# Kernel tuning notes

Measured on AMD Instinct MI355X. Metric: run time of the kernel, lower is better.

The kernel has to match this reference:

```python
import jax, jax.numpy as jnp
import numpy as np
import math

V = 32768; H = 768; NH = 12; D = 64; L = 12; I = 2048
S = 512; B = 8; BK = 32; MAXP = 512; EPS = 1e-7
STD = math.sqrt(2.0 / (5.0 * H))
SCALE = 1.0 / math.sqrt(3 * D)


def _bucket_positions(seq_len):
    # static numpy: DeBERTa-style log-bucketed relative positions
    rel = np.arange(seq_len)[:, None] - np.arange(seq_len)[None, :]
    sign = np.sign(rel)
    mid = BK // 2
    abs_pos = np.where((rel < mid) & (rel > -mid), mid - 1, np.minimum(np.abs(rel), MAXP - 1))
    log_pos = np.ceil(np.log(abs_pos / mid) / math.log((MAXP - 1) / mid) * (mid - 1)).astype(np.int64) + mid
    bucket = np.where(abs_pos <= mid, rel, log_pos * sign).astype(np.int64)
    return bucket + BK - 1  # [S, S] in [0, 2*BK-2]


def _ln(x):
    # LayerNorm without affine params (elementwise_affine=False)
    m = jnp.mean(x, axis=-1, keepdims=True)
    v = jnp.var(x, axis=-1, keepdims=True)
    return (x - m) * jax.lax.rsqrt(v + EPS)


def _forward(input_ids, attention_mask, word_emb, rel_emb, rel_g, rel_b,
             Wqk, bqk, Wvg, bvg, Wout, bout, W1, W2):
    pos_idx = jnp.asarray(_bucket_positions(S))      # [S, S]
    x = _ln(word_emb[input_ids])                     # [S, B, H]
    rel = _ln(rel_emb) * rel_g + rel_b               # [2*BK-1, H] (affine LN)
    mask = attention_mask                            # [B, 1, 1, S] bool, True = masked
    for i in range(L):
        # ---- disentangled attention ----
        hs = _ln(x)
        qk = jnp.einsum('sbh,oh->sbo', hs, Wqk[i]) + bqk[i]
        q, k = jnp.split(qk, 2, axis=-1)
        vg = jnp.einsum('sbh,oh->sbo', hs, Wvg[i]) + bvg[i]
        v, g = jnp.split(vg, 2, axis=-1)
        g = jax.nn.gelu(g, approximate=False)
        pos = jnp.einsum('rh,oh->ro', rel, Wqk[i]) + bqk[i]   # [2*BK-1, 2H]
        posg = pos[pos_idx]                                   # [S, S, 2H]
        qpos, kpos = jnp.split(posg, 2, axis=-1)
        qpos = qpos.reshape(S, S, NH, D)
        kpos = kpos.reshape(S, S, NH, D)
        qh = q.reshape(S, B, NH, D)
        kh = k.reshape(S, B, NH, D)
        vh = v.reshape(S, B, NH, D)
        scores = jnp.einsum('qbhd,kbhd->bhqk', qh, kh) * SCALE          # content-content
        scores = scores + jnp.einsum('qbhd,qkhd->bhqk', qh, kpos) * SCALE  # content-position
        scores = scores + jnp.einsum('kbhd,qkhd->bhqk', kh, qpos) * SCALE  # position-content
        s = jnp.where(mask, -1e9, scores)
        p = jax.nn.softmax(s, axis=-1)
        p = jnp.where(mask, 0.0, p)
        ctx = jnp.einsum('bhqk,kbhd->qbhd', p, vh).reshape(S, B, H)
        ctx = _ln(ctx * g)
        ctx = jnp.einsum('sbh,oh->sbo', ctx, Wout[i]) + bout[i]
        x = x + ctx
        # ---- GeGLU feed-forward ----
        h = _ln(x)
        h = jnp.einsum('sbh,oh->sbo', h, W1[i])   # [S, B, 2I]
        a, gt = jnp.split(h, 2, axis=-1)
        h = _ln(a * jax.nn.gelu(gt, approximate=True))
        h = jnp.einsum('sbi,oi->sbo', h, W2[i])
        x = x + h
    return x


def setup_inputs() -> dict:
    key = jax.random.key(0)
    ks = jax.random.split(key, 12)
    def nrm(k, shape):
        return (jax.random.normal(k, shape) * STD).astype(jnp.float32)
    return {
        'input_ids': jax.random.randint(ks[0], (S, B), 0, V),
        'attention_mask': jax.random.randint(ks[1], (B, 1, 1, S), 0, 2).astype(bool),
        'word_emb': nrm(ks[2], (V, H)),
        'rel_emb': nrm(ks[3], (2 * BK - 1, H)),
        'rel_g': jnp.ones((H,), jnp.float32),
        'rel_b': jnp.zeros((H,), jnp.float32),
        'Wqk': nrm(ks[4], (L, 2 * H, H)),
        'bqk': jnp.zeros((L, 2 * H), jnp.float32),
        'Wvg': nrm(ks[5], (L, 2 * H, H)),
        'bvg': jnp.zeros((L, 2 * H), jnp.float32),
        'Wout': nrm(ks[6], (L, H, H)),
        'bout': jnp.zeros((L, H), jnp.float32),
        'W1': nrm(ks[7], (L, 2 * I, H)),
        'W2': nrm(ks[8], (L, H, I)),
    }


def reference(input_ids, attention_mask, word_emb, rel_emb, rel_g, rel_b,
              Wqk, bqk, Wvg, bvg, Wout, bout, W1, W2):
    return _forward(input_ids, attention_mask, word_emb, rel_emb, rel_g, rel_b,
                    Wqk, bqk, Wvg, bvg, Wout, bout, W1, W2)
```

## Files before the change

kernel.cpp:

```cpp
#include <hip/hip_runtime.h>
#include <math.h>

#define SS 512
#define BB 8
#define NHH 12
#define DD 64
#define HH 768
#define II 2048
#define LL 12
#define SCALE_F 0.07216878364870323f

typedef __attribute__((ext_vector_type(8))) short bf16x8;
typedef __attribute__((ext_vector_type(4))) float f32x4;

__device__ __forceinline__ unsigned short f2b(float f) {
    union { float f; unsigned int u; } x; x.f = f;
    unsigned int r = x.u + 0x7fffu + ((x.u >> 16) & 1u);
    return (unsigned short)(r >> 16);
}
__device__ __forceinline__ float b2f(unsigned short u) {
    union { unsigned int u; float f; } x; x.u = ((unsigned int)u) << 16;
    return x.f;
}

__device__ __forceinline__ float2 blockReduceSum2(float a, float b) {
    __shared__ float2 sm[4];
    __shared__ float2 bc;
#pragma unroll
    for (int o = 32; o > 0; o >>= 1) {
        a += __shfl_down(a, o);
        b += __shfl_down(b, o);
    }
    int t = threadIdx.x;
    if ((t & 63) == 0) sm[t >> 6] = make_float2(a, b);
    __syncthreads();
    if (t == 0) {
        float xa = sm[0].x + sm[1].x + sm[2].x + sm[3].x;
        float xb = sm[0].y + sm[1].y + sm[2].y + sm[3].y;
        bc = make_float2(xa, xb);
    }
    __syncthreads();
    return bc;
}

__device__ __forceinline__ float gelu_erf(float v) {
    return 0.5f * v * (1.0f + erff(v * 0.70710678118654752f));
}
__device__ __forceinline__ float gelu_tanh(float v) {
    const float c = 0.7978845608028654f;
    return 0.5f * v * (1.0f + tanhf(c * (v + 0.044715f * v * v * v)));
}

__global__ __launch_bounds__(256) void k_decode_mask(const unsigned char* __restrict__ raw,
                                                     int* __restrict__ mask, int n) {
    __shared__ int s_any;
    if (threadIdx.x == 0) s_any = 0;
    __syncthreads();
    int local = 0;
    for (int i = threadIdx.x; i < n; i += blockDim.x)
        if ((i & 3) && raw[i]) local = 1;
    if (local) atomicOr(&s_any, 1);
    __syncthreads();
    bool isU8 = (s_any != 0);
    const int* as_int = (const int*)raw;
    for (int i = threadIdx.x; i < n; i += blockDim.x)
        mask[i] = isU8 ? (raw[i] != 0) : (as_int[i] != 0);
}

__global__ __launch_bounds__(256) void k_bucket(int* __restrict__ tab) {
    int i = blockIdx.x * 256 + threadIdx.x;
    if (i >= 1023) return;
    int rel = i - 511;
    int a = rel < 0 ? -rel : rel;
    int abs_pos = (a < 16) ? 15 : (a < 511 ? a : 511);
    int bucket;
    if (abs_pos <= 16) {
        bucket = rel;
    } else {
        double lp = ceil(log((double)abs_pos / 16.0) / log(511.0 / 16.0) * 15.0);
        int l = (int)lp + 16;
        bucket = (rel > 0) ? l : -l;
    }
    int idx = bucket + 31;
    if (idx < 0) idx = 0;
    if (idx > 62) idx = 62;
    tab[i] = idx;
}

__global__ __launch_bounds__(256) void k_f2b(const float* __restrict__ in,
                                             unsigned short* __restrict__ out, int n8) {
    int i = blockIdx.x * 256 + threadIdx.x;
    if (i >= n8) return;
    float4 a = ((const float4*)in)[2 * (size_t)i];
    float4 b = ((const float4*)in)[2 * (size_t)i + 1];
    ushort4 lo, hi;
    lo.x = f2b(a.x); lo.y = f2b(a.y); lo.z = f2b(a.z); lo.w = f2b(a.w);
    hi.x = f2b(b.x); hi.y = f2b(b.y); hi.z = f2b(b.z); hi.w = f2b(b.w);
    ((ushort4*)out)[2 * (size_t)i] = lo;
    ((ushort4*)out)[2 * (size_t)i + 1] = hi;
}

__global__ __launch_bounds__(256) void k_f2b_ln(const float* __restrict__ wvg,
                                                const float* __restrict__ wout,
                                                const float* __restrict__ w1,
                                                const float* __restrict__ w2,
                                                unsigned short* __restrict__ wbf,
                                                const float* __restrict__ x,
                                                unsigned short* __restrict__ hs) {
    int bid = blockIdx.x;
    int t = threadIdx.x;
    if (bid < 3169) {
        int i = bid * 256 + t;
        if (i >= 811008) return;
        const float* src;
        int off;
        if (i < 221184) {
            if (i < 147456) { src = wvg;  off = i; }
            else            { src = wout; off = i - 147456; }
        } else if (i < 614400) { src = w1; off = i - 221184; }
        else                   { src = w2; off = i - 614400; }
        float4 a = ((const float4*)src)[2 * (size_t)off];
        float4 b = ((const float4*)src)[2 * (size_t)off + 1];
        ushort4 lo, hi;
        lo.x = f2b(a.x); lo.y = f2b(a.y); lo.z = f2b(a.z); lo.w = f2b(a.w);
        hi.x = f2b(b.x); hi.y = f2b(b.y); hi.z = f2b(b.z); hi.w = f2b(b.w);
        ((ushort4*)wbf)[2 * (size_t)i] = lo;
        ((ushort4*)wbf)[2 * (size_t)i + 1] = hi;
    } else {
        int row = bid - 3169;
        const float* r = x + (size_t)row * HH;
        float v0 = r[t], v1 = r[t + 256], v2 = r[t + 512];
        float s = v0 + v1 + v2;
        float ss = v0 * v0 + v1 * v1 + v2 * v2;
        float2 r2 = blockReduceSum2(s, ss);
        float mean = r2.x * (1.0f / HH);
        float var = r2.y * (1.0f / HH) - mean * mean;
        float rs = rsqrtf(var + 1e-7f);
        unsigned short* o = hs + (size_t)row * HH;
        o[t] = f2b((v0 - mean) * rs);
        o[t + 256] = f2b((v1 - mean) * rs);
        o[t + 512] = f2b((v2 - mean) * rs);
    }
}

__global__ __launch_bounds__(256) void k_ln_bf(const float* __restrict__ in,
                                               unsigned short* __restrict__ out) {
    int row = blockIdx.x, t = threadIdx.x;
    const float* r = in + (size_t)row * HH;
    float v0 = r[t], v1 = r[t + 256], v2 = r[t + 512];
    float s = v0 + v1 + v2;
    float ss = v0 * v0 + v1 * v1 + v2 * v2;
    float2 r2 = blockReduceSum2(s, ss);
    float mean = r2.x * (1.0f / HH);
    float var = r2.y * (1.0f / HH) - mean * mean;
    float rs = rsqrtf(var + 1e-7f);
    unsigned short* o = out + (size_t)row * HH;
    o[t] = f2b((v0 - mean) * rs);
    o[t + 256] = f2b((v1 - mean) * rs);
    o[t + 512] = f2b((v2 - mean) * rs);
}

__global__ __launch_bounds__(256) void k_embed_ln(const int* __restrict__ ids,
                                                  const float* __restrict__ emb,
                                                  float* __restrict__ out) {
    int row = blockIdx.x, t = threadIdx.x;
    const float* r = emb + (size_t)ids[row] * HH;
    float v0 = r[t], v1 = r[t + 256], v2 = r[t + 512];
    float s = v0 + v1 + v2;
    float ss = v0 * v0 + v1 * v1 + v2 * v2;
    float2 r2 = blockReduceSum2(s, ss);
    float mean = r2.x * (1.0f / HH);
    float var = r2.y * (1.0f / HH) - mean * mean;
    float rs = rsqrtf(var + 1e-7f);
    float* o = out + (size_t)row * HH;
    o[t] = (v0 - mean) * rs;
    o[t + 256] = (v1 - mean) * rs;
    o[t + 512] = (v2 - mean) * rs;
}

__global__ __launch_bounds__(256) void k_rel_ln_bf(const float* __restrict__ rel_emb,
                                                   const float* __restrict__ g,
                                                   const float* __restrict__ b,
                                                   unsigned short* __restrict__ out) {
    int row = blockIdx.x, t = threadIdx.x;
    unsigned short* o = out + (size_t)row * HH;
    if (row >= 63) {
        o[t] = 0; o[t + 256] = 0; o[t + 512] = 0;
        return;
    }
    const float* r = rel_emb + (size_t)row * HH;
    float v0 = r[t], v1 = r[t + 256], v2 = r[t + 512];
    float s = v0 + v1 + v2;
    float ss = v0 * v0 + v1 * v1 + v2 * v2;
    float2 r2 = blockReduceSum2(s, ss);
    float mean = r2.x * (1.0f / HH);
    float var = r2.y * (1.0f / HH) - mean * mean;
    float rs = rsqrtf(var + 1e-7f);
    o[t] = f2b((v0 - mean) * rs * g[t] + b[t]);
    o[t + 256] = f2b((v1 - mean) * rs * g[t + 256] + b[t + 256]);
    o[t + 512] = f2b((v2 - mean) * rs * g[t + 512] + b[t + 512]);
}

__global__ __launch_bounds__(256) void k_gated_ln(const float* __restrict__ ctxr,
                                                  const unsigned short* __restrict__ qkvg,
                                                  unsigned short* __restrict__ out) {
    int row = blockIdx.x, t = threadIdx.x;
    const float* cr = ctxr + (size_t)row * HH;
    const unsigned short* gr = qkvg + (size_t)row * 3072 + 2304;
    float v[3];
    float s = 0.f, ss = 0.f;
#pragma unroll
    for (int e = 0; e < 3; ++e) {
        int i = t + e * 256;
        float x = cr[i] * gelu_erf(b2f(gr[i]));
        v[e] = x;
        s += x; ss += x * x;
    }
    float2 r2 = blockReduceSum2(s, ss);
    float mean = r2.x * (1.0f / HH);
    float var = r2.y * (1.0f / HH) - mean * mean;
    float rs = rsqrtf(var + 1e-7f);
    unsigned short* o = out + (size_t)row * HH;
#pragma unroll
    for (int e = 0; e < 3; ++e) o[t + e * 256] = f2b((v[e] - mean) * rs);
}

__global__ __launch_bounds__(256) void k_ffn_ln(const unsigned short* __restrict__ ffh,
                                                unsigned short* __restrict__ out) {
    int row = blockIdx.x, t = threadIdx.x;
    const unsigned short* ar = ffh + (size_t)row * 4096 + t * 8;
    const unsigned short* gr = ar + II;
    ushort4 a0 = *(const ushort4*)ar;
    ushort4 a1 = *(const ushort4*)(ar + 4);
    ushort4 g0 = *(const ushort4*)gr;
    ushort4 g1 = *(const ushort4*)(gr + 4);
    float av[8] = {b2f(a0.x), b2f(a0.y), b2f(a0.z), b2f(a0.w),
                   b2f(a1.x), b2f(a1.y), b2f(a1.z), b2f(a1.w)};
    float gv[8] = {b2f(g0.x), b2f(g0.y), b2f(g0.z), b2f(g0.w),
                   b2f(g1.x), b2f(g1.y), b2f(g1.z), b2f(g1.w)};
    float v[8];
    float s = 0.f, ss = 0.f;
#pragma unroll
    for (int e = 0; e < 8; ++e) {
        float x = av[e] * gelu_tanh(gv[e]);
        v[e] = x;
        s += x; ss += x * x;
    }
    float2 r2 = blockReduceSum2(s, ss);
    float mean = r2.x * (1.0f / II);
    float var = r2.y * (1.0f / II) - mean * mean;
    float rs = rsqrtf(var + 1e-7f);
    ushort4 o0, o1;
    o0.x = f2b((v[0] - mean) * rs); o0.y = f2b((v[1] - mean) * rs);
    o0.z = f2b((v[2] - mean) * rs); o0.w = f2b((v[3] - mean) * rs);
    o1.x = f2b((v[4] - mean) * rs); o1.y = f2b((v[5] - mean) * rs);
    o1.z = f2b((v[6] - mean) * rs); o1.w = f2b((v[7] - mean) * rs);
    unsigned short* o = out + (size_t)row * II + t * 8;
    *(ushort4*)o = o0;
    *(ushort4*)(o + 4) = o1;
}

template <int OBF>
__global__ __launch_bounds__(256) void k_gemm_bf16(const unsigned short* __restrict__ A, int lda,
                                                   const unsigned short* __restrict__ W, int ldw,
                                                   void* __restrict__ Cv, int ldc,
                                                   int M, int N, int K,
                                                   const float* __restrict__ bias,
                                                   const float* __restrict__ bias2,
                                                   const float* __restrict__ res,
                                                   size_t wz, size_t cz, size_t bz) {
    __shared__ unsigned short As[128 * 32];
    __shared__ unsigned short Ws[128 * 32];
    int zz = blockIdx.z;
    W += (size_t)zz * wz;
    if (bias) bias += (size_t)zz * bz;
    int nwg = gridDim.x * gridDim.y;
    int orig = blockIdx.y * gridDim.x + blockIdx.x;
    int qq = nwg >> 3, rr = nwg & 7;
    int xcd = orig & 7, idx = orig >> 3;
    int wg = (xcd < rr ? xcd * (qq + 1) : rr * (qq + 1) + (xcd - rr) * qq) + idx;
    int bx = wg % gridDim.x, by = wg / gridDim.x;

    const int t = threadIdx.x;
    const int lane = t & 63, wid = t >> 6;
    const int row0 = by * 128, col0 = bx * 128;
    const int wr = (wid >> 1) * 64, wc = (wid & 1) * 64;
    const int rA = lane & 15, kA = (lane >> 4) * 8;

    f32x4 acc[4][4] = {};

    for (int k0 = 0; k0 < K; k0 += 32) {
#pragma unroll
        for (int j = 0; j < 2; ++j) {
            int c = t + j * 256;
            int r = c >> 2, ko = (c & 3) * 8;
            const unsigned short* srcA = A + (size_t)(row0 + r) * lda + k0 + ko;
            const unsigned short* srcB = W + (size_t)(col0 + r) * ldw + k0 + ko;
            unsigned short* dstA = As + (size_t)(j * 256 + wid * 64) * 8;
            unsigned short* dstB = Ws + (size_t)(j * 256 + wid * 64) * 8;
            __builtin_amdgcn_global_load_lds(
                (const __attribute__((address_space(1))) void*)srcA,
                (__attribute__((address_space(3))) void*)dstA, 16, 0, 0);
            __builtin_amdgcn_global_load_lds(
                (const __attribute__((address_space(1))) void*)srcB,
                (__attribute__((address_space(3))) void*)dstB, 16, 0, 0);
        }
        __syncthreads();
        bf16x8 af[4], bfr[4];
#pragma unroll
        for (int m = 0; m < 4; ++m)
            af[m] = *(const bf16x8*)&As[(wr + m * 16 + rA) * 32 + kA];
#pragma unroll
        for (int n = 0; n < 4; ++n)
            bfr[n] = *(const bf16x8*)&Ws[(wc + n * 16 + rA) * 32 + kA];
#pragma unroll
        for (int m = 0; m < 4; ++m)
#pragma unroll
            for (int n = 0; n < 4; ++n)
                acc[m][n] = __builtin_amdgcn_mfma_f32_16x16x32_bf16(af[m], bfr[n], acc[m][n], 0, 0, 0);
        __syncthreads();
    }

    float* Cf = (float*)Cv + (size_t)zz * cz;
    unsigned short* Cb = (unsigned short*)Cv + (size_t)zz * cz;
    const int cl = lane & 15, rg = (lane >> 4) * 4;
#pragma unroll
    for (int n = 0; n < 4; ++n) {
        int gc = col0 + wc + n * 16 + cl;
        float bv = 0.0f;
        if (bias) bv = (bias2 && gc >= 1536) ? bias2[gc - 1536] : bias[gc];
#pragma unroll
        for (int m = 0; m < 4; ++m) {
#pragma unroll
            for (int i = 0; i < 4; ++i) {
                int gr = row0 + wr + m * 16 + rg + i;
                float v = acc[m][n][i] + bv;
                if (OBF) {
                    Cb[(size_t)gr * ldc + gc] = f2b(v);
                } else {
                    if (res) v += res[(size_t)gr * ldc + gc];
                    Cf[(size_t)gr * ldc + gc] = v;
                }
            }
        }
    }
}

#define SKSLOT 16384

__device__ __forceinline__ void sk_stage(const unsigned short* __restrict__ Ab, int lda,
                                         const unsigned short* __restrict__ Wb, int ldw,
                                         unsigned char* slot, int t, int wid) {
    int rit = t >> 3;
    int kb = (t & 7) << 4;
#pragma unroll
    for (int c = 0; c < 2; ++c) {
        int row = c * 32 + rit;
        int gkb = kb ^ ((row & 7) << 4);
        const unsigned short* src = Ab + (size_t)row * lda + (gkb >> 1);
        unsigned char* dst = slot + c * 4096 + wid * 1024;
        __builtin_amdgcn_global_load_lds(
            (const __attribute__((address_space(1))) void*)src,
            (__attribute__((address_space(3))) void*)dst, 16, 0, 0);
    }
#pragma unroll
    for (int c = 0; c < 2; ++c) {
        int row = c * 32 + rit;
        int gkb = kb ^ ((row & 7) << 4);
        const unsigned short* src = Wb + (size_t)row * ldw + (gkb >> 1);
        unsigned char* dst = slot + 8192 + c * 4096 + wid * 1024;
        __builtin_amdgcn_global_load_lds(
            (const __attribute__((address_space(1))) void*)src,
            (__attribute__((address_space(3))) void*)dst, 16, 0, 0);
    }
}

__device__ __forceinline__ void sk_compute(const unsigned char* slot, int wr, int wc,
                                           int rA, int g16, f32x4 acc[2][2]) {
    const unsigned char* Ab = slot;
    const unsigned char* Bb = slot + 8192;
    bf16x8 a[2][2], b[2][2];
#pragma unroll
    for (int m = 0; m < 2; ++m) {
        int row = wr + m * 16 + rA;
        int sw = (row & 7) << 4;
#pragma unroll
        for (int s = 0; s < 2; ++s)
            a[m][s] = *(const bf16x8*)(Ab + row * 128 + ((s * 64 + g16 * 16) ^ sw));
    }
#pragma unroll
    for (int n = 0; n < 2; ++n) {
        int row = wc + n * 16 + rA;
        int sw = (row & 7) << 4;
#pragma unroll
        for (int s = 0; s < 2; ++s)
            b[n][s] = *(const bf16x8*)(Bb + row * 128 + ((s * 64 + g16 * 16) ^ sw));
    }
    __builtin_amdgcn_s_setprio(1);
#pragma unroll
    for (int m = 0; m < 2; ++m)
#pragma unroll
        for (int n = 0; n < 2; ++n) {
            acc[m][n] = __builtin_amdgcn_mfma_f32_16x16x32_bf16(a[m][0], b[n][0], acc[m][n], 0, 0, 0);
            acc[m][n] = __builtin_amdgcn_mfma_f32_16x16x32_bf16(a[m][1], b[n][1], acc[m][n], 0, 0, 0);
        }
    __builtin_amdgcn_s_setprio(0);
}

__global__ __launch_bounds__(256) void k_gemm_skinny(const unsigned short* __restrict__ A, int lda,
                                                     const unsigned short* __restrict__ W, int ldw,
                                                     float* __restrict__ C, int ldc,
                                                     int M, int N, int K,
                                                     const float* __restrict__ bias,
                                                     const float* __restrict__ res) {
    __shared__ unsigned char smem[2 * SKSLOT];
    int nwg = gridDim.x * gridDim.y;
    int orig = blockIdx.y * gridDim.x + blockIdx.x;
    int qq = nwg >> 3, rr = nwg & 7;
    int xcd = orig & 7, idx = orig >> 3;
    int wg = (xcd < rr ? xcd * (qq + 1) : rr * (qq + 1) + (xcd - rr) * qq) + idx;
    int bx = wg % gridDim.x, by = wg / gridDim.x;

    const int t = threadIdx.x;
    const int lane = t & 63, wid = t >> 6;
    const int row0 = by * 64, col0 = bx * 64;
    const int wr = (wid >> 1) * 32, wc = (wid & 1) * 32;
    const int rA = lane & 15, g16 = lane >> 4;
    const unsigned short* Abase = A + (size_t)row0 * lda;
    const unsigned short* Wbase = W + (size_t)col0 * ldw;

    const int nt = K >> 6;
    f32x4 acc[2][2] = {};

    sk_stage(Abase, lda, Wbase, ldw, smem, t, wid);

    for (int tt = 0; tt < nt; ++tt) {
        asm volatile("s_barrier" ::: "memory");
        if (tt + 1 < nt) {
            sk_stage(Abase + (size_t)(tt + 1) * 64, lda, Wbase + (size_t)(tt + 1) * 64,
                     ldw, smem + (size_t)((tt + 1) & 1) * SKSLOT, t, wid);
            asm volatile("s_waitcnt vmcnt(4)" ::: "memory");
        } else {
            asm volatile("s_waitcnt vmcnt(0)" ::: "memory");
        }
        asm volatile("s_barrier" ::: "memory");
        sk_compute(smem + (size_t)(tt & 1) * SKSLOT, wr, wc, rA, g16, acc);
    }

    const int cl = lane & 15, rg = (lane >> 4) * 4;
#pragma unroll
    for (int n = 0; n < 2; ++n) {
        int gc = col0 + wc + n * 16 + cl;
        float bv = bias ? bias[gc] : 0.0f;
#pragma unroll
        for (int m = 0; m < 2; ++m) {
#pragma unroll
            for (int i = 0; i < 4; ++i) {
                int gr = row0 + wr + m * 16 + rg + i;
                float v = acc[m][n][i] + bv;
                if (res) v += res[(size_t)gr * ldc + gc];
                C[(size_t)gr * ldc + gc] = v;
            }
        }
    }
}

#define MDSLOT 32768

__device__ __forceinline__ void md_stage(const unsigned short* __restrict__ Ab, int lda,
                                         const unsigned short* __restrict__ Wb, int ldw,
                                         unsigned char* slot, int t, int wid) {
    int rit = t >> 3;
    int kb = (t & 7) << 4;
#pragma unroll
    for (int c = 0; c < 2; ++c) {
        int row = c * 64 + rit;
        int gkb = kb ^ ((row & 7) << 4);
        const unsigned short* src = Ab + (size_t)row * lda + (gkb >> 1);
        unsigned char* dst = slot + c * 8192 + wid * 1024;
        __builtin_amdgcn_global_load_lds(
            (const __attribute__((address_space(1))) void*)src,
            (__attribute__((address_space(3))) void*)dst, 16, 0, 0);
    }
#pragma unroll
    for (int c = 0; c < 2; ++c) {
        int row = c * 64 + rit;
        int gkb = kb ^ ((row & 7) << 4);
        const unsigned short* src = Wb + (size_t)row * ldw + (gkb >> 1);
        unsigned char* dst = slot + 16384 + c * 8192 + wid * 1024;
        __builtin_amdgcn_global_load_lds(
            (const __attribute__((address_space(1))) void*)src,
            (__attribute__((address_space(3))) void*)dst, 16, 0, 0);
    }
}

__device__ __forceinline__ void md_compute(const unsigned char* slot, int wm, int wn,
                                           int rA, int g16, f32x4 acc[4][2]) {
    const unsigned char* Ab = slot;
    const unsigned char* Bb = slot + 16384;
    bf16x8 a[4][2], b[2][2];
#pragma unroll
    for (int m = 0; m < 4; ++m) {
        int row = wm * 64 + m * 16 + rA;
        int sw = (row & 7) << 4;
#pragma unroll
        for (int s = 0; s < 2; ++s)
            a[m][s] = *(const bf16x8*)(Ab + row * 128 + ((s * 64 + g16 * 16) ^ sw));
    }
#pragma unroll
    for (int n = 0; n < 2; ++n) {
        int row = wn * 32 + n * 16 + rA;
        int sw = (row & 7) << 4;
#pragma unroll
        for (int s = 0; s < 2; ++s)
            b[n][s] = *(const bf16x8*)(Bb + row * 128 + ((s * 64 + g16 * 16) ^ sw));
    }
    __builtin_amdgcn_s_setprio(1);
#pragma unroll
    for (int m = 0; m < 4; ++m)
#pragma unroll
        for (int n = 0; n < 2; ++n) {
            acc[m][n] = __builtin_amdgcn_mfma_f32_16x16x32_bf16(a[m][0], b[n][0], acc[m][n], 0, 0, 0);
            acc[m][n] = __builtin_amdgcn_mfma_f32_16x16x32_bf16(a[m][1], b[n][1], acc[m][n], 0, 0, 0);
        }
    __builtin_amdgcn_s_setprio(0);
}

template <int SCATTER>
__global__ __launch_bounds__(512) void k_gemm_mid(const unsigned short* __restrict__ A, int lda,
                                                  const unsigned short* __restrict__ W,
                                                  const unsigned short* __restrict__ Wb2, int ldw,
                                                  unsigned short* __restrict__ Cb, int ldc,
                                                  int M, int N, int K,
                                                  const float* __restrict__ bias,
                                                  const float* __restrict__ bias2,
                                                  unsigned short* __restrict__ qT,
                                                  unsigned short* __restrict__ kT) {
    extern __shared__ unsigned char smem[];
    int nwg = gridDim.x * gridDim.y;
    int orig = blockIdx.y * gridDim.x + blockIdx.x;
    int qq = nwg >> 3, rr = nwg & 7;
    int xcd = orig & 7, idx = orig >> 3;
    int wg = (xcd < rr ? xcd * (qq + 1) : rr * (qq + 1) + (xcd - rr) * qq) + idx;
    int bx = wg % gridDim.x, by = wg / gridDim.x;

    const int t = threadIdx.x;
    const int lane = t & 63, wid = t >> 6;
    const int wm = wid >> 2, wn = wid & 3;
    const int rA = lane & 15, g16 = lane >> 4;
    const int row0 = by * 128, col0 = bx * 128;
    const unsigned short* Abase = A + (size_t)row0 * lda;
    const unsigned short* Wbase = (Wb2 && col0 >= 1536)
                                      ? Wb2 + (size_t)(col0 - 1536) * ldw
                                      : W + (size_t)col0 * ldw;

    const int nt = K >> 6;
    f32x4 acc[4][2] = {};

    md_stage(Abase, lda, Wbase, ldw, smem, t, wid);

    for (int tt = 0; tt < nt; ++tt) {
        asm volatile("s_barrier" ::: "memory");
        if (tt + 1 < nt) {
            md_stage(Abase + (size_t)(tt + 1) * 64, lda, Wbase + (size_t)(tt + 1) * 64,
                     ldw, smem + (size_t)((tt + 1) & 1) * MDSLOT, t, wid);
            asm volatile("s_waitcnt vmcnt(4)" ::: "memory");
        } else {
            asm volatile("s_waitcnt vmcnt(0)" ::: "memory");
        }
        asm volatile("s_barrier" ::: "memory");
        md_compute(smem + (size_t)(tt & 1) * MDSLOT, wm, wn, rA, g16, acc);
    }

    const int cl = lane & 15, rg = (lane >> 4) * 4;
#pragma unroll
    for (int n = 0; n < 2; ++n) {
        int gc = col0 + wn * 32 + n * 16 + cl;
        float bv = 0.0f;
        if (bias) bv = (bias2 && gc >= 1536) ? bias2[gc - 1536] : bias[gc];
        if (SCATTER && gc < 1536) {
            int isk = gc >= HH;
            unsigned short* dst = isk ? kT : qT;
            int h = (isk ? gc - HH : gc) >> 6;
            int d = gc & 63;
#pragma unroll
            for (int m = 0; m < 4; ++m) {
#pragma unroll
                for (int i = 0; i < 4; ++i) {
                    int gr = row0 + wm * 64 + m * 16 + rg + i;
                    int s = gr >> 3, b = gr & 7;
                    dst[(((size_t)(b * NHH + h)) * SS + s) * DD + d] = f2b(acc[m][n][i] + bv);
                }
            }
        } else {
#pragma unroll
            for (int m = 0; m < 4; ++m) {
#pragma unroll
                for (int i = 0; i < 4; ++i) {
                    int gr = row0 + wm * 64 + m * 16 + rg + i;
                    Cb[(size_t)gr * ldc + gc] = f2b(acc[m][n][i] + bv);
                }
            }
        }
    }
}

__global__ __launch_bounds__(256) void k_repack_cppc(const unsigned short* __restrict__ qkvg,
                                                     const unsigned short* __restrict__ pp,
                                                     const unsigned short* __restrict__ qT,
                                                     const unsigned short* __restrict__ kT,
                                                     unsigned short* __restrict__ vT,
                                                     float* __restrict__ cp,
                                                     float* __restrict__ pc) {
    __shared__ unsigned char shmem[12288];
    int t = threadIdx.x;
    if (blockIdx.x < 8) {
        unsigned short (*tile)[72] = (unsigned short(*)[72])shmem;
        int bh = blockIdx.y;
        int b = bh / NHH, h = bh % NHH;
        int s0 = blockIdx.x * 64;
#pragma unroll
        for (int j = 0; j < 4; ++j) {
            int idx = t + j * 256;
            int r = idx >> 4, c4 = idx & 15;
            ushort4 u = *(const ushort4*)(qkvg + ((size_t)(s0 + r) * BB + b) * 3072 + 1536 + h * DD + c4 * 4);
            *(ushort4*)&tile[r][c4 * 4] = u;
        }
        __syncthreads();
#pragma unroll
        for (int j = 0; j < 2; ++j) {
            int idx = t + j * 256;
            int d = idx >> 3, s8 = idx & 7;
            ushort4 a, c;
            a.x = tile[s8 * 8 + 0][d]; a.y = tile[s8 * 8 + 1][d];
            a.z = tile[s8 * 8 + 2][d]; a.w = tile[s8 * 8 + 3][d];
            c.x = tile[s8 * 8 + 4][d]; c.y = tile[s8 * 8 + 5][d];
            c.z = tile[s8 * 8 + 6][d]; c.w = tile[s8 * 8 + 7][d];
            unsigned short* dst = vT + ((size_t)bh * DD + d) * SS + s0 + s8 * 8;
            *(ushort4*)dst = a; *(ushort4*)(dst + 4) = c;
        }
    } else {
        int cid = (blockIdx.x - 8) * 96 + blockIdx.y;
        int z = cid >= 384;
        int rem = cid - (z ? 384 : 0);
        int h = rem >> 5;
        int mt = rem & 31;
        int toff = z ? 0 : HH;
        float* out = z ? pc : cp;
        const unsigned short* srcbase = z ? kT : qT;
        unsigned short* As = (unsigned short*)shmem;
        unsigned short* Bs = (unsigned short*)(shmem + 8192);
        const int lane = t & 63, wid = t >> 6;
        const int rA = lane & 15, kA = (lane >> 4) * 8;

        f32x4 acc[2][4] = {};

        for (int k0 = 0; k0 < 64; k0 += 32) {
#pragma unroll
            for (int j = 0; j < 2; ++j) {
                int c = t + j * 256;
                int r = c >> 2, ko = (c & 3) * 8;
                int row = mt * 128 + r;
                int s = row >> 3, b = row & 7;
                const unsigned short* srcA =
                    srcbase + (((size_t)(b * NHH + h)) * SS + s) * DD + k0 + ko;
                unsigned short* dstA = As + (size_t)(j * 256 + wid * 64) * 8;
                __builtin_amdgcn_global_load_lds(
                    (const __attribute__((address_space(1))) void*)srcA,
                    (__attribute__((address_space(3))) void*)dstA, 16, 0, 0);
            }
            {
                int r = t >> 2, ko = (t & 3) * 8;
                const unsigned short* srcB = pp + (size_t)r * 1536 + toff + h * DD + k0 + ko;
                unsigned short* dstB = Bs + (size_t)(wid * 64) * 8;
                __builtin_amdgcn_global_load_lds(
                    (const __attribute__((address_space(1))) void*)srcB,
                    (__attribute__((address_space(3))) void*)dstB, 16, 0, 0);
            }
            __syncthreads();
            bf16x8 af[2], bfr[4];
#pragma unroll
            for (int m = 0; m < 2; ++m)
                af[m] = *(const bf16x8*)&As[(wid * 32 + m * 16 + rA) * 32 + kA];
#pragma unroll
            for (int n = 0; n < 4; ++n)
                bfr[n] = *(const bf16x8*)&Bs[(n * 16 + rA) * 32 + kA];
#pragma unroll
            for (int m = 0; m < 2; ++m)
#pragma unroll
                for (int n = 0; n < 4; ++n)
                    acc[m][n] = __builtin_amdgcn_mfma_f32_16x16x32_bf16(af[m], bfr[n], acc[m][n], 0, 0, 0);
            __syncthreads();
        }

        const int cl = lane & 15, rg = (lane >> 4) * 4;
#pragma unroll
        for (int m = 0; m < 2; ++m)
#pragma unroll
            for (int n = 0; n < 4; ++n) {
                int gc = n * 16 + cl;
                if (gc < 63) {
#pragma unroll
                    for (int i = 0; i < 4; ++i) {
                        int gr = mt * 128 + wid * 32 + m * 16 + rg + i;
                        int sIdx = gr >> 3, bIdx = gr & 7;
                        out[(((size_t)(bIdx * NHH + h)) * SS + sIdx) * 63 + gc] = acc[m][n][i];
                    }
                }
            }
    }
}

__global__ __launch_bounds__(256) void k_attn_fused(
    const unsigned short* __restrict__ qT, const unsigned short* __restrict__ kT,
    const unsigned short* __restrict__ vT, const float* __restrict__ cp,
    const float* __restrict__ pc, const int* __restrict__ bucket,
    const int* __restrict__ mask, float* __restrict__ ctxr) {
    __shared__ float cps[64 * 63];
    __shared__ float pcs[64 * 63];
    __shared__ unsigned short pb_all[4][16 * 72];
    __shared__ int btab[1023];
    int t = threadIdx.x;
    int lane = t & 63, wid = t >> 6;
    int bh = blockIdx.y;
    int b = bh / NHH, h = bh % NHH;
    int qb0 = blockIdx.x * 64;
    int q0 = qb0 + wid * 16;
    int rA = lane & 15, g = lane >> 4, kA = g * 8;
    unsigned short* pb = pb_all[wid];
    const unsigned short* qTb = qT + (size_t)bh * SS * DD;
    const unsigned short* kTb = kT + (size_t)bh * SS * DD;
    const unsigned short* vTb = vT + (size_t)bh * DD * SS;
    const float* cpb = cp + (size_t)bh * SS * 63 + (size_t)qb0 * 63;
    const float* pcb = pc + (size_t)bh * SS * 63;
    const int* mkb = mask + b * SS;

    for (int i = t; i < 1023; i += 256) btab[i] = bucket[i];
    for (int i = t; i < 1008; i += 256) ((float4*)cps)[i] = ((const float4*)cpb)[i];

    bf16x8 aq[2];
#pragma unroll
    for (int dc = 0; dc < 2; ++dc)
        aq[dc] = *(const bf16x8*)&qTb[(size_t)(q0 + rA) * DD + dc * 32 + kA];

    f32x4 o[4] = {};
    float lrow[4];
#pragma unroll
    for (int i = 0; i < 4; ++i) lrow[i] = 0.f;

    for (int kt = 0; kt < 8; ++kt) {
        int k0 = kt * 64;
        __syncthreads();
        {
            const float4* src = (const float4*)(pcb + (size_t)k0 * 63);
            for (int i = t; i < 1008; i += 256) ((float4*)pcs)[i] = src[i];
        }
        f32x4 sa[4] = {};
#pragma unroll
        for (int n = 0; n < 4; ++n) {
            bf16x8 bk0 = *(const bf16x8*)&kTb[(size_t)(k0 + n * 16 + rA) * DD + kA];
            bf16x8 bk1 = *(const bf16x8*)&kTb[(size_t)(k0 + n * 16 + rA) * DD + 32 + kA];
            sa[n] = __builtin_amdgcn_mfma_f32_16x16x32_bf16(aq[0], bk0, sa[n], 0, 0, 0);
            sa[n] = __builtin_amdgcn_mfma_f32_16x16x32_bf16(aq[1], bk1, sa[n], 0, 0, 0);
        }
        int mk[4];
#pragma unroll
        for (int n = 0; n < 4; ++n) mk[n] = mkb[k0 + n * 16 + rA];
        __syncthreads();

        float pv[4][4];
#pragma unroll
        for (int i = 0; i < 4; ++i) {
            int qr = wid * 16 + g * 4 + i;
            int q = qb0 + qr;
            float ls = 0.f;
#pragma unroll
            for (int n = 0; n < 4; ++n) {
                int kr = n * 16 + rA;
                int id = btab[q - (k0 + kr) + 511];
                float v = (sa[n][i] + cps[qr * 63 + id] + pcs[kr * 63 + id]) * SCALE_F;
                v = mk[n] ? -1e9f : v;
                float p = __expf(v);
                pv[n][i] = p;
                ls += p;
            }
            ls += __shfl_xor(ls, 1, 16);
            ls += __shfl_xor(ls, 2, 16);
            ls += __shfl_xor(ls, 4, 16);
            ls += __shfl_xor(ls, 8, 16);
            lrow[i] += ls;
        }
#pragma unroll
        for (int n = 0; n < 4; ++n)
#pragma unroll
            for (int i = 0; i < 4; ++i)
                pb[(g * 4 + i) * 72 + n * 16 + rA] = f2b(pv[n][i]);
        bf16x8 ap[2];
#pragma unroll
        for (int kc = 0; kc < 2; ++kc)
            ap[kc] = *(const bf16x8*)&pb[rA * 72 + kc * 32 + kA];
#pragma unroll
        for (int n = 0; n < 4; ++n) {
            bf16x8 bv0 = *(const bf16x8*)&vTb[(size_t)(n * 16 + rA) * SS + k0 + kA];
            bf16x8 bv1 = *(const bf16x8*)&vTb[(size_t)(n * 16 + rA) * SS + k0 + 32 + kA];
            o[n] = __builtin_amdgcn_mfma_f32_16x16x32_bf16(ap[0], bv0, o[n], 0, 0, 0);
            o[n] = __builtin_amdgcn_mfma_f32_16x16x32_bf16(ap[1], bv1, o[n], 0, 0, 0);
        }
    }
#pragma unroll
    for (int i = 0; i < 4; ++i) {
        int q = q0 + g * 4 + i;
        float inv = 1.0f / lrow[i];
#pragma unroll
        for (int n = 0; n < 4; ++n)
            ctxr[((size_t)q * BB + b) * HH + h * DD + n * 16 + rA] = o[n][i] * inv;
    }
}

extern "C" void kernel_launch(void* const* d_in, const int* in_sizes, int n_in,
                              void* d_out, int out_size, void* d_ws, size_t ws_size,
                              hipStream_t stream) {
    static int attr_done = 0;
    if (!attr_done) {
        hipFuncSetAttribute((const void*)&k_gemm_mid<0>,
                            hipFuncAttributeMaxDynamicSharedMemorySize, 2 * MDSLOT);
        hipFuncSetAttribute((const void*)&k_gemm_mid<1>,
                            hipFuncAttributeMaxDynamicSharedMemorySize, 2 * MDSLOT);
        attr_done = 1;
    }

    const int* ids = (const int*)d_in[0];
    const unsigned char* maskraw = (const unsigned char*)d_in[1];
    const float* word_emb = (const float*)d_in[2];
    const float* rel_emb = (const float*)d_in[3];
    const float* rel_g = (const float*)d_in[4];
    const float* rel_b = (const float*)d_in[5];
    const float* Wqk = (const float*)d_in[6];
    const float* bqk = (const float*)d_in[7];
    const float* Wvg = (const float*)d_in[8];
    const float* bvg = (const float*)d_in[9];
    const float* Wout = (const float*)d_in[10];
    const float* bout = (const float*)d_in[11];
    const float* W1 = (const float*)d_in[12];
    const float* W2 = (const float*)d_in[13];

    const size_t N_X = (size_t)SS * BB * HH;
    const size_t N_CP = (size_t)SS * BB * NHH * 63;
    const size_t N_H2 = (size_t)SS * BB * II;
    const size_t N_WQK = (size_t)2 * HH * HH;
    const size_t N_WOUT = (size_t)HH * HH;
    const size_t N_W1 = (size_t)2 * II * HH;
    const size_t N_W2 = (size_t)HH * II;
    const size_t N_HD = (size_t)BB * NHH * SS * DD;
    const size_t N_QKVG = (size_t)SS * BB * 3072;
    const size_t N_FFH = (size_t)SS * BB * 4096;
    const size_t N_PP = (size_t)128 * 1536;

    float* ws = (float*)d_ws;
    float* x = ws;
    float* ctxr = x + N_X;
    float* cp = ctxr + N_X;
    float* pc = cp + N_CP;
    unsigned short* us = (unsigned short*)(pc + N_CP);
    unsigned short* qkvg = us;
    unsigned short* hs_bf = qkvg + N_QKVG;
    unsigned short* ctx_bf = hs_bf + N_X;
    unsigned short* h2_bf = ctx_bf + N_X;
    unsigned short* ffh = h2_bf + N_H2;
    unsigned short* wqk_all = ffh + N_FFH;
    unsigned short* wvg_bf = wqk_all + 12 * N_WQK;
    unsigned short* wout_bf = wvg_bf + N_WQK;
    unsigned short* w1_bf = wout_bf + N_WOUT;
    unsigned short* w2_bf = w1_bf + N_W1;
    unsigned short* ppall = w2_bf + N_W2;
    unsigned short* rel_bf = ppall + 12 * N_PP;
    unsigned short* qT = rel_bf + 128 * HH;
    unsigned short* kT = qT + N_HD;
    unsigned short* vT = kT + N_HD;
    int* bucket = (int*)(vT + N_HD);
    int* maski = bucket + 1024;

    size_t need_bytes = ((size_t)(maski + BB * SS) - (size_t)d_ws);
    if (ws_size < need_bytes) return;

    k_decode_mask<<<1, 256, 0, stream>>>(maskraw, maski, BB * SS);
    k_bucket<<<4, 256, 0, stream>>>(bucket);
    k_embed_ln<<<SS * BB, 256, 0, stream>>>(ids, word_emb, x);
    k_rel_ln_bf<<<128, 256, 0, stream>>>(rel_emb, rel_g, rel_b, rel_bf);
    k_f2b<<<(int)((12 * N_WQK / 8 + 255) / 256), 256, 0, stream>>>(Wqk, wqk_all,
                                                                   (int)(12 * N_WQK / 8));
    {
        dim3 gpp(1536 / 128, 1, 12);
        k_gemm_bf16<1><<<gpp, 256, 0, stream>>>(rel_bf, HH, wqk_all, HH, ppall, 1536,
                                                128, 1536, HH, bqk, nullptr, nullptr,
                                                N_WQK, N_PP, 2 * HH);
    }

    for (int l = 0; l < LL; ++l) {
        const unsigned short* wqk_l = wqk_all + (size_t)l * N_WQK;
        const float* bqk_l = bqk + (size_t)l * 2 * HH;
        const float* Wvg_l = Wvg + (size_t)l * N_WQK;
        const float* bvg_l = bvg + (size_t)l * 2 * HH;
        const float* Wout_l = Wout + (size_t)l * N_WOUT;
        const float* bout_l = bout + (size_t)l * HH;
        const float* W1_l = W1 + (size_t)l * N_W1;
        const float* W2_l = W2 + (size_t)l * N_W2;

        k_f2b_ln<<<3169 + SS * BB, 256, 0, stream>>>(Wvg_l, Wout_l, W1_l, W2_l, wvg_bf,
                                                     x, hs_bf);
        {
            dim3 g(3072 / 128, SS * BB / 128);
            k_gemm_mid<1><<<g, 512, 2 * MDSLOT, stream>>>(hs_bf, HH, wqk_l, wvg_bf, HH,
                                                          qkvg, 3072, SS * BB, 3072, HH,
                                                          bqk_l, bvg_l, qT, kT);
        }
        k_repack_cppc<<<dim3(16, 96), 256, 0, stream>>>(qkvg, ppall + (size_t)l * N_PP,
                                                        qT, kT, vT, cp, pc);
        k_attn_fused<<<dim3(SS / 64, BB * NHH), 256, 0, stream>>>(qT, kT, vT, cp, pc,
                                                                  bucket, maski, ctxr);
        k_gated_ln<<<SS * BB, 256, 0, stream>>>(ctxr, qkvg, ctx_bf);
        k_gemm_skinny<<<dim3(HH / 64, SS * BB / 64), 256, 0, stream>>>(
            ctx_bf, HH, wout_bf, HH, x, HH, SS * BB, HH, HH, bout_l, x);

        k_ln_bf<<<SS * BB, 256, 0, stream>>>(x, hs_bf);
        {
            dim3 g(4096 / 128, SS * BB / 128);
            k_gemm_mid<0><<<g, 512, 2 * MDSLOT, stream>>>(hs_bf, HH, w1_bf, nullptr, HH,
                                                          ffh, 4096, SS * BB, 4096, HH,
                                                          nullptr, nullptr, nullptr, nullptr);
        }
        k_ffn_ln<<<SS * BB, 256, 0, stream>>>(ffh, h2_bf);
        float* outC = (l == LL - 1) ? (float*)d_out : x;
        k_gemm_skinny<<<dim3(HH / 64, SS * BB / 64), 256, 0, stream>>>(
            h2_bf, II, w2_bf, II, outC, HH, SS * BB, HH, II, nullptr, x);
    }
}
```

Measured before the change: 2.630 ms.

## Replace skinny GEMM with 128x64 tile, 8-wave, triple-buffered n64 GEMM

After: 2.598 ms. About the same (-1.2%).

```diff
diff --git a/kernel.cpp b/kernel.cpp
--- a/kernel.cpp
+++ b/kernel.cpp
@@ -346,43 +346,42 @@
     }
 }
 
-#define SKSLOT 16384
-
-__device__ __forceinline__ void sk_stage(const unsigned short* __restrict__ Ab, int lda,
-                                         const unsigned short* __restrict__ Wb, int ldw,
-                                         unsigned char* slot, int t, int wid) {
+#define N64SLOT 24576
+
+__device__ __forceinline__ void n64_stage(const unsigned short* __restrict__ Ab, int lda,
+                                          const unsigned short* __restrict__ Wb, int ldw,
+                                          unsigned char* slot, int t, int wid) {
     int rit = t >> 3;
     int kb = (t & 7) << 4;
 #pragma unroll
     for (int c = 0; c < 2; ++c) {
-        int row = c * 32 + rit;
+        int row = c * 64 + rit;
         int gkb = kb ^ ((row & 7) << 4);
         const unsigned short* src = Ab + (size_t)row * lda + (gkb >> 1);
-        unsigned char* dst = slot + c * 4096 + wid * 1024;
+        unsigned char* dst = slot + c * 8192 + wid * 1024;
         __builtin_amdgcn_global_load_lds(
             (const __attribute__((address_space(1))) void*)src,
             (__attribute__((address_space(3))) void*)dst, 16, 0, 0);
     }
-#pragma unroll
-    for (int c = 0; c < 2; ++c) {
-        int row = c * 32 + rit;
+    {
+        int row = rit;
         int gkb = kb ^ ((row & 7) << 4);
         const unsigned short* src = Wb + (size_t)row * ldw + (gkb >> 1);
-        unsigned char* dst = slot + 8192 + c * 4096 + wid * 1024;
+        unsigned char* dst = slot + 16384 + wid * 1024;
         __builtin_amdgcn_global_load_lds(
             (const __attribute__((address_space(1))) void*)src,
             (__attribute__((address_space(3))) void*)dst, 16, 0, 0);
     }
 }
 
-__device__ __forceinline__ void sk_compute(const unsigned char* slot, int wr, int wc,
-                                           int rA, int g16, f32x4 acc[2][2]) {
+__device__ __forceinline__ void n64_compute(const unsigned char* slot, int wm, int wn,
+                                            int rA, int g16, f32x4 acc[2][2]) {
     const unsigned char* Ab = slot;
-    const unsigned char* Bb = slot + 8192;
+    const unsigned char* Bb = slot + 16384;
     bf16x8 a[2][2], b[2][2];
 #pragma unroll
     for (int m = 0; m < 2; ++m) {
-        int row = wr + m * 16 + rA;
+        int row = wm * 32 + m * 16 + rA;
         int sw = (row & 7) << 4;
 #pragma unroll
         for (int s = 0; s < 2; ++s)
@@ -390,7 +389,7 @@
     }
 #pragma unroll
     for (int n = 0; n < 2; ++n) {
-        int row = wc + n * 16 + rA;
+        int row = wn * 32 + n * 16 + rA;
         int sw = (row & 7) << 4;
 #pragma unroll
         for (int s = 0; s < 2; ++s)
@@ -407,13 +406,13 @@
     __builtin_amdgcn_s_setprio(0);
 }
 
-__global__ __launch_bounds__(256) void k_gemm_skinny(const unsigned short* __restrict__ A, int lda,
-                                                     const unsigned short* __restrict__ W, int ldw,
-                                                     float* __restrict__ C, int ldc,
-                                                     int M, int N, int K,
-                                                     const float* __restrict__ bias,
-                                                     const float* __restrict__ res) {
-    __shared__ unsigned char smem[2 * SKSLOT];
+__global__ __launch_bounds__(512) void k_gemm_n64(const unsigned short* __restrict__ A, int lda,
+                                                  const unsigned short* __restrict__ W, int ldw,
+                                                  float* __restrict__ C, int ldc,
+                                                  int M, int N, int K,
+                                                  const float* __restrict__ bias,
+                                                  const float* __restrict__ res) {
+    extern __shared__ unsigned char smem[];
     int nwg = gridDim.x * gridDim.y;
     int orig = blockIdx.y * gridDim.x + blockIdx.x;
     int qq = nwg >> 3, rr = nwg & 7;
@@ -423,40 +422,48 @@
 
     const int t = threadIdx.x;
     const int lane = t & 63, wid = t >> 6;
-    const int row0 = by * 64, col0 = bx * 64;
-    const int wr = (wid >> 1) * 32, wc = (wid & 1) * 32;
+    const int wm = wid >> 1, wn = wid & 1;
     const int rA = lane & 15, g16 = lane >> 4;
+    const int row0 = by * 128, col0 = bx * 64;
     const unsigned short* Abase = A + (size_t)row0 * lda;
     const unsigned short* Wbase = W + (size_t)col0 * ldw;
 
     const int nt = K >> 6;
     f32x4 acc[2][2] = {};
 
-    sk_stage(Abase, lda, Wbase, ldw, smem, t, wid);
-
-    for (int tt = 0; tt < nt; ++tt) {
-        asm volatile("s_barrier" ::: "memory");
-        if (tt + 1 < nt) {
-            sk_stage(Abase + (size_t)(tt + 1) * 64, lda, Wbase + (size_t)(tt + 1) * 64,
-                     ldw, smem + (size_t)((tt + 1) & 1) * SKSLOT, t, wid);
-            asm volatile("s_waitcnt vmcnt(4)" ::: "memory");
-        } else {
-            asm volatile("s_waitcnt vmcnt(0)" ::: "memory");
-        }
-        asm volatile("s_barrier" ::: "memory");
-        sk_compute(smem + (size_t)(tt & 1) * SKSLOT, wr, wc, rA, g16, acc);
-    }
+    n64_stage(Abase, lda, Wbase, ldw, smem, t, wid);
+    n64_stage(Abase + 64, lda, Wbase + 64, ldw, smem + N64SLOT, t, wid);
+
+#define NBAR() asm volatile("s_barrier" ::: "memory")
+#define NITER(T, STG, VMSTR)                                                         \
+    do {                                                                             \
+        NBAR();        \
+        if (STG)                                                                     \
+            n64_stage(Abase + (size_t)(T + 2) * 64, lda, Wbase + (size_t)(T + 2) * 64,\
+                      ldw, smem + (size_t)((T + 2) % 3) * N64SLOT, t, wid);          \
+        asm volatile(VMSTR ::: "memory");              \
+        NBAR();                                     \
+        n64_compute(smem + (size_t)((T) % 3) * N64SLOT, wm, wn, rA, g16, acc);       \
+    } while (0)
+
+    int tt = 0;
+    for (; tt < nt - 2; ++tt) NITER(tt, true, "s_waitcnt vmcnt(6)");
+    NITER(tt, false, "s_waitcnt vmcnt(3)");
+    ++tt;
+    NITER(tt, false, "s_waitcnt vmcnt(0)");
+#undef NITER
+#undef NBAR
 
     const int cl = lane & 15, rg = (lane >> 4) * 4;
 #pragma unroll
     for (int n = 0; n < 2; ++n) {
-        int gc = col0 + wc + n * 16 + cl;
+        int gc = col0 + wn * 32 + n * 16 + cl;
         float bv = bias ? bias[gc] : 0.0f;
 #pragma unroll
         for (int m = 0; m < 2; ++m) {
 #pragma unroll
             for (int i = 0; i < 4; ++i) {
-                int gr = row0 + wr + m * 16 + rg + i;
+                int gr = row0 + wm * 32 + m * 16 + rg + i;
                 float v = acc[m][n][i] + bv;
                 if (res) v += res[(size_t)gr * ldc + gc];
                 C[(size_t)gr * ldc + gc] = v;
@@ -826,6 +833,8 @@
                             hipFuncAttributeMaxDynamicSharedMemorySize, 2 * MDSLOT);
         hipFuncSetAttribute((const void*)&k_gemm_mid<1>,
                             hipFuncAttributeMaxDynamicSharedMemorySize, 2 * MDSLOT);
+        hipFuncSetAttribute((const void*)&k_gemm_n64,
+                            hipFuncAttributeMaxDynamicSharedMemorySize, 3 * N64SLOT);
         attr_done = 1;
     }
 
@@ -919,7 +928,7 @@
         k_attn_fused<<<dim3(SS / 64, BB * NHH), 256, 0, stream>>>(qT, kT, vT, cp, pc,
                                                                   bucket, maski, ctxr);
         k_gated_ln<<<SS * BB, 256, 0, stream>>>(ctxr, qkvg, ctx_bf);
-        k_gemm_skinny<<<dim3(HH / 64, SS * BB / 64), 256, 0, stream>>>(
+        k_gemm_n64<<<dim3(HH / 64, SS * BB / 128), 512, 3 * N64SLOT, stream>>>(
             ctx_bf, HH, wout_bf, HH, x, HH, SS * BB, HH, HH, bout_l, x);
 
         k_ln_bf<<<SS * BB, 256, 0, stream>>>(x, hs_bf);
@@ -931,7 +940,7 @@
         }
         k_ffn_ln<<<SS * BB, 256, 0, stream>>>(ffh, h2_bf);
         float* outC = (l == LL - 1) ? (float*)d_out : x;
-        k_gemm_skinny<<<dim3(HH / 64, SS * BB / 64), 256, 0, stream>>>(
+        k_gemm_n64<<<dim3(HH / 64, SS * BB / 128), 512, 3 * N64SLOT, stream>>>(
             h2_bf, II, w2_bf, II, outC, HH, SS * BB, HH, II, nullptr, x);
     }
 }
```
